# Kernel tuning notes

Hardware: AMD Instinct MI355X
Metric: run time of the kernel (lower is better)

The kernel has to match this reference:

```python
import jax, jax.numpy as jnp
import numpy as np

STEP = 1.0  # module init arg
N = 8192


def setup_inputs() -> dict:
    key = jax.random.key(0)
    k1, = jax.random.split(key, 1)
    predictions = jax.random.normal(k1, (N, 1), dtype=jnp.float32) * 50.0  # depth-like values
    z_spacing = jnp.ones((), dtype=jnp.float32) * 2.5
    nth_slice = jnp.ones((), dtype=jnp.float32) * 4.0
    return {"predictions": predictions, "z_spacing": z_spacing, "nth_slice": nth_slice}


def reference(predictions, z_spacing, nth_slice):
    p = predictions[:, 0]                       # [N]
    n = p.shape[0]
    acceptable_step = STEP * z_spacing * nth_slice
    # closed form of the loop-built step matrix: steps[i,j] = |i-j| * acceptable_step
    idx = jnp.arange(n)
    steps = jnp.abs(idx[:, None] - idx[None, :]).astype(p.dtype) * acceptable_step  # [N,N]
    d = p[:, None] - p[None, :]                 # [N,N] pairwise differences
    # first masked update: where d >= 0, subtract 0.2*steps
    d = jnp.where(d >= 0, d - 0.2 * steps, d)
    # second masked update on the updated d: clamp (d - 0.8*steps) at 0
    d = jnp.where(d >= 0, jnp.maximum(d - 0.8 * steps, jnp.zeros((), d.dtype)), d)
    loss = jnp.sum(jnp.abs(jnp.tril(d))) / (n * n)
    return loss
```

## Files before the change

### kernel.cpp

```cpp
#include <hip/hip_runtime.h>


constexpr int ROWS = 256;
constexpr int COLS = 128;

__global__ __launch_bounds__(ROWS) void depth_loss_kernel(
    const float* __restrict__ p,
    const float* __restrict__ zsp,
    const float* __restrict__ nsl,
    double* __restrict__ partials)
{
    int b = blockIdx.x;
    int ri = (int)((sqrtf(4.0f * (float)b + 1.0f) - 1.0f) * 0.5f);
    while ((ri + 1) * (ri + 2) <= b) ++ri;
    while (ri * (ri + 1) > b) --ri;
    int cj = b - ri * (ri + 1);

    int tid = threadIdx.x;
    int i = ri * ROWS + tid;
    float pi = p[i];

    __shared__ __align__(16) float pj[COLS];
    int jbase = cj * COLS;
    if (tid < COLS / 4)
        ((float4*)pj)[tid] = ((const float4*)(p + jbase))[tid];
    __syncthreads();

    float a   = zsp[0] * nsl[0];
    float a02 = 0.2f * a;
    float dij = (float)(i - jbase);

    float acc0 = 0.0f, acc1 = 0.0f;
    const float4* pj4 = (const float4*)pj;

#define PAIR_BODY(PJV, ACC, MASKED)                                \
    {                                                              \
        float n0 = (PJV) - pi;                                     \
        float e1 = __builtin_fmaf(dij, a02, n0);    \
        float t  = __builtin_fmaf(dij, a,   n0);    \
        float cp = fmaxf(fmaxf(e1, -t), 0.0f);      \
        float c  = (n0 > 0.0f) ? n0 : cp;                          \
        if (MASKED) c = (dij >= 0.0f) ? c : 0.0f;                  \
        ACC += c;                                                  \
        dij -= 1.0f;                                               \
    }

    if (cj < 2 * ri) {
        #pragma unroll 8
        for (int q = 0; q < COLS / 4; ++q) {
            float4 v = pj4[q];
            PAIR_BODY(v.x, acc0, false)
            PAIR_BODY(v.y, acc1, false)
            PAIR_BODY(v.z, acc0, false)
            PAIR_BODY(v.w, acc1, false)
        }
    } else {
        #pragma unroll 8
        for (int q = 0; q < COLS / 4; ++q) {
            float4 v = pj4[q];
            PAIR_BODY(v.x, acc0, true)
            PAIR_BODY(v.y, acc1, true)
            PAIR_BODY(v.z, acc0, true)
            PAIR_BODY(v.w, acc1, true)
        }
    }
#undef PAIR_BODY

    float acc = acc0 + acc1;

    for (int off = 32; off > 0; off >>= 1)
        acc += __shfl_down(acc, off, 64);

    __shared__ float wsum[ROWS / 64];
    if ((tid & 63) == 0) wsum[tid >> 6] = acc;
    __syncthreads();

    if (tid == 0) {
        float blocksum = 0.0f;
        for (int w = 0; w < ROWS / 64; ++w) blocksum += wsum[w];
        partials[blockIdx.x] = (double)blocksum;
    }
}

__global__ __launch_bounds__(256) void finalize_kernel(
    const double* __restrict__ partials, int nblocks, float* __restrict__ out,
    double inv_nn)
{
    int tid = threadIdx.x;
    double acc = 0.0;
    for (int b = tid; b < nblocks; b += 256) acc += partials[b];
    for (int off = 32; off > 0; off >>= 1)
        acc += __shfl_down(acc, off, 64);
    __shared__ double wsum[4];
    if ((tid & 63) == 0) wsum[tid >> 6] = acc;
    __syncthreads();
    if (tid == 0)
        out[0] = (float)((wsum[0] + wsum[1] + wsum[2] + wsum[3]) * inv_nn);
}

extern "C" void kernel_launch(void* const* d_in, const int* in_sizes, int n_in,
                              void* d_out, int out_size, void* d_ws, size_t ws_size,
                              hipStream_t stream) {
    const float* p   = (const float*)d_in[0];
    const float* zsp = (const float*)d_in[1];
    const float* nsl = (const float*)d_in[2];
    float* out = (float*)d_out;
    double* partials = (double*)d_ws;

    int n = in_sizes[0];
    int nrt = (n + ROWS - 1) / ROWS;
    int nblocks = nrt * (nrt + 1);
    double inv_nn = 1.0 / ((double)n * (double)n);

    depth_loss_kernel<<<nblocks, ROWS, 0, stream>>>(p, zsp, nsl, partials);
    finalize_kernel<<<1, 256, 0, stream>>>(partials, nblocks, out, inv_nn);
}
```

Before: 68.28 us.

## Vectorize pair loss with packed f32x2 math and halve column tile

```diff
diff --git a/kernel.cpp b/kernel.cpp
--- a/kernel.cpp
+++ b/kernel.cpp
@@ -1,8 +1,10 @@
 #include <hip/hip_runtime.h>
 
 
+typedef float f32x2 __attribute__((ext_vector_type(2)));
+
 constexpr int ROWS = 256;
-constexpr int COLS = 128;
+constexpr int COLS = 64;
 
 __global__ __launch_bounds__(ROWS) void depth_loss_kernel(
     const float* __restrict__ p,
@@ -11,10 +13,10 @@
     double* __restrict__ partials)
 {
     int b = blockIdx.x;
-    int ri = (int)((sqrtf(4.0f * (float)b + 1.0f) - 1.0f) * 0.5f);
-    while ((ri + 1) * (ri + 2) <= b) ++ri;
-    while (ri * (ri + 1) > b) --ri;
-    int cj = b - ri * (ri + 1);
+    int ri = (int)((sqrtf(2.0f * (float)b + 1.0f) - 1.0f) * 0.5f);
+    while (2 * (ri + 1) * (ri + 2) <= b) ++ri;
+    while (2 * ri * (ri + 1) > b) --ri;
+    int cj = b - 2 * ri * (ri + 1);
 
     int tid = threadIdx.x;
     int i = ri * ROWS + tid;
@@ -28,45 +30,59 @@
 
     float a   = zsp[0] * nsl[0];
     float a02 = 0.2f * a;
-    float dij = (float)(i - jbase);
+    f32x2 av   = { a,   a   };
+    f32x2 a02v = { a02, a02 };
+    f32x2 four = { 4.0f, 4.0f };
+    f32x2 zero = { 0.0f, 0.0f };
+    f32x2 pi2  = { pi, pi };
 
-    float acc0 = 0.0f, acc1 = 0.0f;
+    float dij0 = (float)(i - jbase);
+    f32x2 d2a = { dij0,        dij0 - 1.0f };
+    f32x2 d2b = { dij0 - 2.0f, dij0 - 3.0f };
+
+    f32x2 acc2a = zero, acc2b = zero;
     const float4* pj4 = (const float4*)pj;
 
-#define PAIR_BODY(PJV, ACC, MASKED)                                \
-    {                                                              \
-        float n0 = (PJV) - pi;                                     \
-        float e1 = __builtin_fmaf(dij, a02, n0);    \
-        float t  = __builtin_fmaf(dij, a,   n0);    \
-        float cp = fmaxf(fmaxf(e1, -t), 0.0f);      \
-        float c  = (n0 > 0.0f) ? n0 : cp;                          \
-        if (MASKED) c = (dij >= 0.0f) ? c : 0.0f;                  \
-        ACC += c;                                                  \
-        dij -= 1.0f;                                               \
+#define GROUP_BODY(VA, D2, ACC, MASKED)                               \
+    {                                                                 \
+        f32x2 n0 = (VA) - pi2;                         \
+        f32x2 e1 = __builtin_elementwise_fma(D2, a02v, n0);           \
+        f32x2 t  = __builtin_elementwise_fma(D2, av,   n0);           \
+        f32x2 cp = __builtin_elementwise_max(                         \
+                       __builtin_elementwise_max(e1, -t), zero);      \
+        f32x2 c;                                                      \
+        c.x = (n0.x > 0.0f) ? n0.x : cp.x;                            \
+        c.y = (n0.y > 0.0f) ? n0.y : cp.y;                            \
+        if (MASKED) {                                                 \
+            c.x = (D2.x >= 0.0f) ? c.x : 0.0f;                        \
+            c.y = (D2.y >= 0.0f) ? c.y : 0.0f;                        \
+        }                                                             \
+        ACC += c;                                       \
+        D2  -= four;                                    \
     }
 
-    if (cj < 2 * ri) {
-        #pragma unroll 8
+    if (cj < 4 * ri) {
+        #pragma unroll
         for (int q = 0; q < COLS / 4; ++q) {
             float4 v = pj4[q];
-            PAIR_BODY(v.x, acc0, false)
-            PAIR_BODY(v.y, acc1, false)
-            PAIR_BODY(v.z, acc0, false)
-            PAIR_BODY(v.w, acc1, false)
+            f32x2 va = { v.x, v.y };
+            f32x2 vb = { v.z, v.w };
+            GROUP_BODY(va, d2a, acc2a, false)
+            GROUP_BODY(vb, d2b, acc2b, false)
         }
     } else {
-        #pragma unroll 8
+        #pragma unroll
         for (int q = 0; q < COLS / 4; ++q) {
             float4 v = pj4[q];
-            PAIR_BODY(v.x, acc0, true)
-            PAIR_BODY(v.y, acc1, true)
-            PAIR_BODY(v.z, acc0, true)
-            PAIR_BODY(v.w, acc1, true)
+            f32x2 va = { v.x, v.y };
+            f32x2 vb = { v.z, v.w };
+            GROUP_BODY(va, d2a, acc2a, true)
+            GROUP_BODY(vb, d2b, acc2b, true)
         }
     }
-#undef PAIR_BODY
+#undef GROUP_BODY
 
-    float acc = acc0 + acc1;
+    float acc = (acc2a.x + acc2a.y) + (acc2b.x + acc2b.y);
 
     for (int off = 32; off > 0; off >>= 1)
         acc += __shfl_down(acc, off, 64);
@@ -109,7 +125,7 @@
 
     int n = in_sizes[0];
     int nrt = (n + ROWS - 1) / ROWS;
-    int nblocks = nrt * (nrt + 1);
+    int nblocks = 2 * nrt * (nrt + 1);
     double inv_nn = 1.0 / ((double)n * (double)n);
 
     depth_loss_kernel<<<nblocks, ROWS, 0, stream>>>(p, zsp, nsl, partials);
```

New measurement: 68.01 us. About the same (-0.4%).
